# Performance work log

Hardware: AMD Instinct MI355X
Metric: run time of the kernel (lower is better)

Reference implementation:

```python
import jax, jax.numpy as jnp
import numpy as np

B, CIN, H, W = 4, 256, 64, 64
COUT = CIN // 2  # 128
EPS = 1e-5


def setup_inputs() -> dict:
    key = jax.random.key(0)
    ks = jax.random.split(key, 10)
    s_in = 1.0 / np.sqrt(CIN)
    s_out = 1.0 / np.sqrt(COUT)
    return {
        "x": jax.random.normal(ks[0], (B, CIN, H, W), dtype=jnp.float32),
        "Wq": jax.random.uniform(ks[1], (COUT, CIN), jnp.float32, -s_in, s_in),
        "bq": jax.random.uniform(ks[2], (COUT,), jnp.float32, -s_in, s_in),
        "Wk": jax.random.uniform(ks[3], (COUT, CIN), jnp.float32, -s_in, s_in),
        "bk": jax.random.uniform(ks[4], (COUT,), jnp.float32, -s_in, s_in),
        "Wv": jax.random.uniform(ks[5], (COUT, CIN), jnp.float32, -s_in, s_in),
        "bv": jax.random.uniform(ks[6], (COUT,), jnp.float32, -s_in, s_in),
        "Ww": jax.random.uniform(ks[7], (CIN, COUT), jnp.float32, -s_out, s_out),
        "bw": jax.random.uniform(ks[8], (CIN,), jnp.float32, -s_out, s_out),
        "bn_gamma": jnp.ones((CIN,), jnp.float32),
        "bn_beta": jnp.zeros((CIN,), jnp.float32),
        "bn_mean": jnp.zeros((CIN,), jnp.float32),
        "bn_var": jnp.ones((CIN,), jnp.float32),
    }


def reference(x, Wq, bq, Wk, bk, Wv, bv, Ww, bw, bn_gamma, bn_beta, bn_mean, bn_var):
    b, c, h, w = x.shape
    n = h * w
    xf = x.reshape(b, c, n)  # [B, Cin, N]
    # 1x1 convs == channel-mixing matmuls on flattened spatial dim
    q = jnp.einsum("oc,bcn->bon", Wq, xf) + bq[None, :, None]  # [B, Cout, N]
    k = jnp.einsum("oc,bcn->bon", Wk, xf) + bk[None, :, None]
    v = jnp.einsum("oc,bcn->bon", Wv, xf) + bv[None, :, None]
    # f = k^T @ q  (no scaling, as in the original)
    f = jnp.einsum("bcn,bcm->bnm", k, q)  # [B, N, N]
    f = jax.nn.softmax(f, axis=-1)
    # y = v @ f
    y = jnp.einsum("bcn,bnm->bcm", v, f)  # [B, Cout, N]
    # output 1x1 conv + eval-mode BatchNorm + residual
    z = jnp.einsum("oc,bcn->bon", Ww, y) + bw[None, :, None]  # [B, Cin, N]
    inv = bn_gamma / jnp.sqrt(bn_var + EPS)
    z = z * inv[None, :, None] + (bn_beta - bn_mean * inv)[None, :, None]
    return z.reshape(b, c, h, w) + x
```

## Files before the change

### kernel.cpp

```cpp
#include <hip/hip_runtime.h>
#include <hip/hip_bf16.h>

#define BATCH 4
#define CIN   256
#define CMID  128
#define NPOS  4096
#define EPS   1e-5f

typedef __bf16 bf16;
typedef __attribute__((ext_vector_type(8))) __bf16 bf16x8;
typedef __attribute__((ext_vector_type(4))) __bf16 bf16x4;
typedef __attribute__((ext_vector_type(4))) float  f32x4;

#define MFMA16(a, b, c) __builtin_amdgcn_mfma_f32_16x16x32_bf16((a), (b), (c), 0, 0, 0)

#define GLDS(gsrc, ldst) \
    __builtin_amdgcn_global_load_lds( \
        (const __attribute__((address_space(1))) void*)(gsrc), \
        (__attribute__((address_space(3))) void*)(ldst), 16, 0, 0)

__device__ __forceinline__ int swz128(int row, int colb) {
    return row * 128 + ((((colb >> 4) ^ (row & 7)) << 4) | (colb & 15));
}
__device__ __forceinline__ int swz256(int row, int colb) {
    return row * 256 + ((((colb >> 4) ^ (row & 7)) << 4) | (colb & 15));
}

__global__ __launch_bounds__(256) void kt_transpose(const float* __restrict__ x,
                                                    bf16* __restrict__ xT) {
    __shared__ float tile[64][65];
    int n0 = blockIdx.x * 64, c0 = blockIdx.y * 64, b = blockIdx.z;
    const float* xp = x + (size_t)b * CIN * NPOS;
    int t = threadIdx.x;
    int lr = t >> 4;
    int lc4 = (t & 15) * 4;
    for (int p = 0; p < 4; ++p) {
        int c = lr + p * 16;
        f32x4 v = *reinterpret_cast<const f32x4*>(xp + (size_t)(c0 + c) * NPOS + n0 + lc4);
        tile[c][lc4 + 0] = v[0]; tile[c][lc4 + 1] = v[1];
        tile[c][lc4 + 2] = v[2]; tile[c][lc4 + 3] = v[3];
    }
    __syncthreads();
    bf16* xtp = xT + (size_t)b * NPOS * CIN;
    int cc = (t & 15) * 4;
    for (int p = 0; p < 4; ++p) {
        int n = (t >> 4) + p * 16;
        bf16x4 o;
        o[0] = (bf16)tile[cc + 0][n]; o[1] = (bf16)tile[cc + 1][n];
        o[2] = (bf16)tile[cc + 2][n]; o[3] = (bf16)tile[cc + 3][n];
        *reinterpret_cast<bf16x4*>(xtp + (size_t)(n0 + n) * CIN + c0 + cc) = o;
    }
}

__global__ __launch_bounds__(256) void k_qkv(
    const float* __restrict__ Wq, const float* __restrict__ Wk, const float* __restrict__ Wv,
    const float* __restrict__ bq, const float* __restrict__ bk, const float* __restrict__ bv,
    const bf16* __restrict__ xT, bf16* __restrict__ qT, bf16* __restrict__ kT,
    bf16* __restrict__ vC) {
    __shared__ __align__(16) char a_lds[128 * 128];
    __shared__ __align__(16) char b_lds[128 * 128];
    int n0 = blockIdx.x * 128, which = blockIdx.y, b = blockIdx.z;
    const float* W    = which == 0 ? Wq : (which == 1 ? Wk : Wv);
    const float* bias = which == 0 ? bq : (which == 1 ? bk : bv);
    int t = threadIdx.x, lane = t & 63, w = t >> 6, wy = w >> 1, wx = w & 1;
    const bf16* xb = xT + (size_t)b * NPOS * CIN;

    f32x4 acc[4][4] = {};
    for (int k0 = 0; k0 < 256; k0 += 64) {
        __syncthreads();
        for (int i = 0; i < 8; ++i) {
            int idx = t + i * 256;
            int row = idx >> 4, c4 = (idx & 15) * 4;
            f32x4 v = *reinterpret_cast<const f32x4*>(W + (size_t)row * CIN + k0 + c4);
            bf16x4 o; o[0] = (bf16)v[0]; o[1] = (bf16)v[1]; o[2] = (bf16)v[2]; o[3] = (bf16)v[3];
            *reinterpret_cast<bf16x4*>(a_lds + swz128(row, c4 * 2)) = o;
        }
        for (int i = 0; i < 4; ++i) {
            int idx = t + i * 256;
            int row = idx >> 3, cb = (idx & 7) * 16;
            bf16x8 vv = *reinterpret_cast<const bf16x8*>(xb + (size_t)(n0 + row) * CIN + k0 + cb / 2);
            *reinterpret_cast<bf16x8*>(b_lds + swz128(row, cb)) = vv;
        }
        __syncthreads();
        for (int ks = 0; ks < 2; ++ks) {
            int kb = ks * 64 + (lane >> 4) * 16;
            bf16x8 af[4], bfr[4];
            for (int i = 0; i < 4; ++i)
                af[i] = *reinterpret_cast<const bf16x8*>(a_lds + swz128(wy * 64 + i * 16 + (lane & 15), kb));
            for (int j = 0; j < 4; ++j)
                bfr[j] = *reinterpret_cast<const bf16x8*>(b_lds + swz128(wx * 64 + j * 16 + (lane & 15), kb));
            for (int i = 0; i < 4; ++i)
                for (int j = 0; j < 4; ++j)
                    acc[i][j] = MFMA16(af[i], bfr[j], acc[i][j]);
        }
    }
    int rg = lane >> 4, cl = lane & 15;
    for (int i = 0; i < 4; ++i) {
        int ch0 = wy * 64 + i * 16 + rg * 4;
        f32x4 bv4 = *reinterpret_cast<const f32x4*>(bias + ch0);
        for (int j = 0; j < 4; ++j) {
            int n = n0 + wx * 64 + j * 16 + cl;
            f32x4 d = acc[i][j];
            for (int r = 0; r < 4; ++r) d[r] += bv4[r];
            if (which == 2) {
                for (int r = 0; r < 4; ++r)
                    vC[((size_t)b * CMID + ch0 + r) * NPOS + n] = (bf16)d[r];
            } else {
                bf16x4 o; o[0] = (bf16)d[0]; o[1] = (bf16)d[1]; o[2] = (bf16)d[2]; o[3] = (bf16)d[3];
                bf16* dst = (which == 0 ? qT : kT);
                *reinterpret_cast<bf16x4*>(dst + ((size_t)b * NPOS + n) * CMID + ch0) = o;
            }
        }
    }
}

__global__ __launch_bounds__(256, 4) void k_zrow(const bf16* __restrict__ qT,
                                                 const bf16* __restrict__ kT,
                                                 float* __restrict__ zpart) {
    __shared__ __align__(16) char q_lds[2][64 * 256];
    int n0 = blockIdx.x * 128, mq = blockIdx.y, b = blockIdx.z;
    int t = threadIdx.x, lane = t & 63, w = t >> 6;
    int cl = lane & 15, g = lane >> 4;
    const bf16* qb = qT + (size_t)b * NPOS * CMID;
    const bf16* kb = kT + (size_t)b * NPOS * CMID;

    auto stage_q = [&](int buf, int m0) {
        #pragma unroll
        for (int i = 0; i < 4; ++i) {
            int lc = (w * 4 + i) * 64 + lane;
            int r = lc >> 4, p = lc & 15;
            GLDS(qb + (size_t)(m0 + r) * CMID + ((p ^ (r & 7)) << 3),
                 q_lds[buf] + (w * 4 + i) * 1024);
        }
    };

    bf16x8 kreg[2][4];
    for (int jn = 0; jn < 2; ++jn)
        for (int ks = 0; ks < 4; ++ks)
            kreg[jn][ks] = *reinterpret_cast<const bf16x8*>(
                kb + (size_t)(n0 + w * 32 + jn * 16 + cl) * CMID + ks * 32 + g * 8);

    int mbeg = mq * (NPOS / 8);
    stage_q(0, mbeg);
    asm volatile("s_waitcnt vmcnt(0)" ::: "memory");
    __syncthreads();
    int cur = 0;
    float zacc[2] = {0.f, 0.f};
    for (int m0 = mbeg; m0 < mbeg + NPOS / 8; m0 += 64) {
        if (m0 + 64 < mbeg + NPOS / 8) stage_q(cur ^ 1, m0 + 64);
        f32x4 acc[4][2] = {};
        for (int ks = 0; ks < 4; ++ks) {
            bf16x8 qf[4];
            for (int im = 0; im < 4; ++im)
                qf[im] = *reinterpret_cast<const bf16x8*>(q_lds[cur] + swz256(im * 16 + cl, ks * 64 + g * 16));
            for (int im = 0; im < 4; ++im)
                for (int jn = 0; jn < 2; ++jn)
                    acc[im][jn] = MFMA16(qf[im], kreg[jn][ks], acc[im][jn]);
        }
        for (int im = 0; im < 4; ++im)
            for (int jn = 0; jn < 2; ++jn)
                for (int r = 0; r < 4; ++r)
                    zacc[jn] += __expf(acc[im][jn][r]);
        __syncthreads();
        cur ^= 1;
    }
    for (int jn = 0; jn < 2; ++jn) {
        zacc[jn] += __shfl_xor(zacc[jn], 16);
        zacc[jn] += __shfl_xor(zacc[jn], 32);
    }
    if (g == 0) {
        float* zp = zpart + ((size_t)mq * BATCH + b) * NPOS;
        zp[n0 + w * 32 + cl]      = zacc[0];
        zp[n0 + w * 32 + 16 + cl] = zacc[1];
    }
}

__global__ __launch_bounds__(256) void k_rcp(const float* __restrict__ zpart,
                                             float* __restrict__ invZ) {
    int i = (blockIdx.x * 256 + threadIdx.x) * 4;
    f32x4 s = {0.f, 0.f, 0.f, 0.f};
    for (int p = 0; p < 8; ++p) {
        f32x4 a = *reinterpret_cast<const f32x4*>(zpart + (size_t)p * BATCH * NPOS + i);
        for (int r = 0; r < 4; ++r) s[r] += a[r];
    }
    f32x4 o;
    for (int r = 0; r < 4; ++r) o[r] = 1.f / s[r];
    *reinterpret_cast<f32x4*>(invZ + i) = o;
}

__global__ __launch_bounds__(256) void k_vscale(bf16* __restrict__ vC,
                                                const float* __restrict__ invZ) {
    int idx = blockIdx.x * 256 + threadIdx.x;
    int b = idx >> 16;
    int n8 = idx & (NPOS / 8 - 1);
    bf16x8 v = *reinterpret_cast<const bf16x8*>(vC + (size_t)idx * 8);
    const float* iz = invZ + (size_t)b * NPOS + n8 * 8;
    f32x4 i0 = *reinterpret_cast<const f32x4*>(iz);
    f32x4 i1 = *reinterpret_cast<const f32x4*>(iz + 4);
    bf16x8 o;
    for (int r = 0; r < 4; ++r) {
        o[r]     = (bf16)((float)v[r]     * i0[r]);
        o[r + 4] = (bf16)((float)v[r + 4] * i1[r]);
    }
    *reinterpret_cast<bf16x8*>(vC + (size_t)idx * 8) = o;
}

__global__ __launch_bounds__(256, 2) void k_attn(const bf16* __restrict__ qT,
                                                 const bf16* __restrict__ kT,
                                                 const bf16* __restrict__ vS,
                                                 bf16* __restrict__ ypA,
                                                 bf16* __restrict__ ypB) {
    __shared__ __align__(16) char k_lds[2][64 * 256];
    __shared__ __align__(16) char v_lds[2][128 * 128];
    __shared__ __align__(16) char p_lds[128 * 128];
    int m0 = blockIdx.x * 128, nq = blockIdx.y, b = blockIdx.z;
    int t = threadIdx.x, lane = t & 63, w = t >> 6;
    int cl = lane & 15, g = lane >> 4;
    const bf16* qb = qT + (size_t)b * NPOS * CMID;
    const bf16* kb = kT + (size_t)b * NPOS * CMID;
    const bf16* vb = vS + (size_t)b * CMID * NPOS;

    auto stage_kv = [&](int buf, int n0) {
        #pragma unroll
        for (int i = 0; i < 4; ++i) {
            int lc = (w * 4 + i) * 64 + lane;
            int kr = lc >> 4, kp = lc & 15;
            GLDS(kb + (size_t)(n0 + kr) * CMID + ((kp ^ (kr & 7)) << 3),
                 k_lds[buf] + (w * 4 + i) * 1024);
            int vr = lc >> 3, vp = lc & 7;
            GLDS(vb + (size_t)vr * NPOS + n0 + ((vp ^ (vr & 7)) << 3),
                 v_lds[buf] + (w * 4 + i) * 1024);
        }
    };

    bf16x8 qreg[2][4];
    for (int jm = 0; jm < 2; ++jm)
        for (int ks = 0; ks < 4; ++ks)
            qreg[jm][ks] = *reinterpret_cast<const bf16x8*>(
                qb + (size_t)(m0 + w * 32 + jm * 16 + cl) * CMID + ks * 32 + g * 8);

    f32x4 acc2[2][8] = {};
    int nbeg = nq * (NPOS / 4);
    stage_kv(0, nbeg);
    asm volatile("s_waitcnt vmcnt(0)" ::: "memory");
    __syncthreads();
    int cur = 0;
    for (int s = 0; s < NPOS / 4 / 64; ++s) {
        int n0 = nbeg + s * 64;
        if (s + 1 < NPOS / 4 / 64) stage_kv(cur ^ 1, n0 + 64);
        f32x4 acc1[4][2] = {};
        for (int ks = 0; ks < 4; ++ks) {
            bf16x8 kf[4];
            for (int in = 0; in < 4; ++in)
                kf[in] = *reinterpret_cast<const bf16x8*>(k_lds[cur] + swz256(in * 16 + cl, ks * 64 + g * 16));
            for (int in = 0; in < 4; ++in)
                for (int jm = 0; jm < 2; ++jm)
                    acc1[in][jm] = MFMA16(kf[in], qreg[jm][ks], acc1[in][jm]);
        }
        for (int in = 0; in < 4; ++in)
            for (int jm = 0; jm < 2; ++jm) {
                bf16x4 o;
                for (int r = 0; r < 4; ++r) o[r] = (bf16)__expf(acc1[in][jm][r]);
                *reinterpret_cast<bf16x4*>(p_lds + swz128(w * 32 + jm * 16 + cl, in * 32 + g * 8)) = o;
            }
        for (int s32 = 0; s32 < 2; ++s32) {
            bf16x8 af[2], vf[8];
            for (int jm = 0; jm < 2; ++jm)
                af[jm] = *reinterpret_cast<const bf16x8*>(p_lds + swz128(w * 32 + jm * 16 + cl, s32 * 64 + g * 16));
            for (int j = 0; j < 8; ++j)
                vf[j] = *reinterpret_cast<const bf16x8*>(v_lds[cur] + swz128(j * 16 + cl, s32 * 64 + g * 16));
            for (int jm = 0; jm < 2; ++jm)
                for (int j = 0; j < 8; ++j)
                    acc2[jm][j] = MFMA16(af[jm], vf[j], acc2[jm][j]);
        }
        __syncthreads();
        cur ^= 1;
    }
    bf16* yb = ((nq & 2) ? ypB : ypA) + ((size_t)(nq & 1) * BATCH + b) * NPOS * CMID
             + (size_t)m0 * CMID;
    for (int jm = 0; jm < 2; ++jm)
        for (int j = 0; j < 8; ++j) {
            int c = j * 16 + cl;
            for (int r = 0; r < 4; ++r) {
                int m = w * 32 + jm * 16 + g * 4 + r;
                yb[(size_t)m * CMID + c] = (bf16)acc2[jm][j][r];
            }
        }
}

__global__ __launch_bounds__(256) void k_out(
    const float* __restrict__ Ww, const float* __restrict__ bw,
    const float* __restrict__ gamma, const float* __restrict__ beta,
    const float* __restrict__ mean, const float* __restrict__ var,
    const bf16* __restrict__ ypA, const bf16* __restrict__ ypB,
    const float* __restrict__ x, float* __restrict__ out) {
    __shared__ __align__(16) char a_lds[128 * 128];
    __shared__ __align__(16) char b_lds[128 * 128];
    int m0 = blockIdx.x * 128, o0 = blockIdx.y * 128, b = blockIdx.z;
    int t = threadIdx.x, lane = t & 63, w = t >> 6, wy = w >> 1, wx = w & 1;
    size_t boff = (size_t)b * NPOS * CMID;
    const bf16* y0 = ypA + boff;
    const bf16* y1 = ypA + (size_t)BATCH * NPOS * CMID + boff;
    const bf16* y2 = ypB + boff;
    const bf16* y3 = ypB + (size_t)BATCH * NPOS * CMID + boff;
    f32x4 acc[4][4] = {};
    for (int k0 = 0; k0 < 128; k0 += 64) {
        __syncthreads();
        for (int i = 0; i < 8; ++i) {
            int idx = t + i * 256, row = idx >> 4, c4 = (idx & 15) * 4;
            f32x4 v = *reinterpret_cast<const f32x4*>(Ww + (size_t)(o0 + row) * CMID + k0 + c4);
            bf16x4 o; o[0] = (bf16)v[0]; o[1] = (bf16)v[1]; o[2] = (bf16)v[2]; o[3] = (bf16)v[3];
            *reinterpret_cast<bf16x4*>(a_lds + swz128(row, c4 * 2)) = o;
        }
        for (int i = 0; i < 8; ++i) {
            int idx = t + i * 256, row = idx >> 4, c4 = (idx & 15) * 4;
            size_t yoff = (size_t)(m0 + row) * CMID + k0 + c4;
            bf16x4 a0 = *reinterpret_cast<const bf16x4*>(y0 + yoff);
            bf16x4 a1 = *reinterpret_cast<const bf16x4*>(y1 + yoff);
            bf16x4 a2 = *reinterpret_cast<const bf16x4*>(y2 + yoff);
            bf16x4 a3 = *reinterpret_cast<const bf16x4*>(y3 + yoff);
            bf16x4 o;
            for (int r = 0; r < 4; ++r)
                o[r] = (bf16)((float)a0[r] + (float)a1[r] + (float)a2[r] + (float)a3[r]);
            *reinterpret_cast<bf16x4*>(b_lds + swz128(row, c4 * 2)) = o;
        }
        __syncthreads();
        for (int ks = 0; ks < 2; ++ks) {
            int kb = ks * 64 + (lane >> 4) * 16;
            bf16x8 af[4], bfr[4];
            for (int i = 0; i < 4; ++i)
                af[i] = *reinterpret_cast<const bf16x8*>(a_lds + swz128(wy * 64 + i * 16 + (lane & 15), kb));
            for (int j = 0; j < 4; ++j)
                bfr[j] = *reinterpret_cast<const bf16x8*>(b_lds + swz128(wx * 64 + j * 16 + (lane & 15), kb));
            for (int i = 0; i < 4; ++i)
                for (int j = 0; j < 4; ++j)
                    acc[i][j] = MFMA16(af[i], bfr[j], acc[i][j]);
        }
    }
    int rg = lane >> 4, cl = lane & 15;
    const float* xb = x + (size_t)b * CIN * NPOS;
    float* ob = out + (size_t)b * CIN * NPOS;
    for (int i = 0; i < 4; ++i) {
        int och0 = o0 + wy * 64 + i * 16 + rg * 4;
        f32x4 g  = *reinterpret_cast<const f32x4*>(gamma + och0);
        f32x4 be = *reinterpret_cast<const f32x4*>(beta + och0);
        f32x4 mu = *reinterpret_cast<const f32x4*>(mean + och0);
        f32x4 va = *reinterpret_cast<const f32x4*>(var + och0);
        f32x4 bb = *reinterpret_cast<const f32x4*>(bw + och0);
        float invv[4], addv[4];
        for (int r = 0; r < 4; ++r) {
            invv[r] = g[r] / sqrtf(va[r] + EPS);
            addv[r] = be[r] - mu[r] * invv[r];
        }
        for (int j = 0; j < 4; ++j) {
            int m = m0 + wx * 64 + j * 16 + cl;
            for (int r = 0; r < 4; ++r) {
                float z = (acc[i][j][r] + bb[r]) * invv[r] + addv[r];
                ob[(size_t)(och0 + r) * NPOS + m] = z + xb[(size_t)(och0 + r) * NPOS + m];
            }
        }
    }
}

extern "C" void kernel_launch(void* const* d_in, const int* in_sizes, int n_in,
                              void* d_out, int out_size, void* d_ws, size_t ws_size,
                              hipStream_t stream) {
    const float* x     = (const float*)d_in[0];
    const float* Wq    = (const float*)d_in[1];
    const float* bq    = (const float*)d_in[2];
    const float* Wk    = (const float*)d_in[3];
    const float* bk    = (const float*)d_in[4];
    const float* Wv    = (const float*)d_in[5];
    const float* bv    = (const float*)d_in[6];
    const float* Ww    = (const float*)d_in[7];
    const float* bw    = (const float*)d_in[8];
    const float* gamma = (const float*)d_in[9];
    const float* beta  = (const float*)d_in[10];
    const float* mean  = (const float*)d_in[11];
    const float* var   = (const float*)d_in[12];
    float* out = (float*)d_out;

    char* ws = (char*)d_ws;
    char* regionA = ws;                    ws += (size_t)BATCH * NPOS * CIN * 2;
    bf16* qT = (bf16*)ws;                  ws += (size_t)BATCH * NPOS * CMID * 2;
    bf16* kT = (bf16*)ws;                  ws += (size_t)BATCH * NPOS * CMID * 2;
    bf16* vC = (bf16*)ws;                  ws += (size_t)BATCH * NPOS * CMID * 2;
    bf16* ypB = (bf16*)ws;                 ws += (size_t)2 * BATCH * NPOS * CMID * 2;
    float* zpart = (float*)ws;             ws += (size_t)8 * BATCH * NPOS * 4;
    float* invZ = (float*)ws;
    bf16* xT  = (bf16*)regionA;
    bf16* ypA = (bf16*)regionA;

    kt_transpose<<<dim3(NPOS / 64, CIN / 64, BATCH), 256, 0, stream>>>(x, xT);
    k_qkv<<<dim3(NPOS / 128, 3, BATCH), 256, 0, stream>>>(Wq, Wk, Wv, bq, bk, bv, xT, qT, kT, vC);
    k_zrow<<<dim3(NPOS / 128, 8, BATCH), 256, 0, stream>>>(qT, kT, zpart);
    k_rcp<<<dim3(BATCH * NPOS / 1024), 256, 0, stream>>>(zpart, invZ);
    k_vscale<<<dim3(BATCH * CMID * NPOS / 8 / 256), 256, 0, stream>>>(vC, invZ);
    k_attn<<<dim3(NPOS / 128, 4, BATCH), 256, 0, stream>>>(qT, kT, vC, ypA, ypB);
    k_out<<<dim3(NPOS / 128, 2, BATCH), 256, 0, stream>>>(Ww, bw, gamma, beta, mean, var, ypA, ypB, x, out);
}
```

Measured before the change: 99.81 us.

## Triple-buffer K/V and Q tiles with 32-row stages and finer output tiling

The zrow and attention kernels move from double-buffered 64-row stages to triple-buffered 32-row stages. Each stage waits with a partial vmcnt and a single barrier, and the MFMA sections run at raised priority through setprio. The V tile layout and the P scratch layout change to a 4-chunk XOR swizzle that matches the 32-wide K step. The output kernel uses 64-column tiles, which doubles the grid for better occupancy. The smaller stages add more barriers and loop iterations, and LDS per block shrinks.

```diff
diff --git a/kernel.cpp b/kernel.cpp
--- a/kernel.cpp
+++ b/kernel.cpp
@@ -19,11 +19,16 @@
         (const __attribute__((address_space(1))) void*)(gsrc), \
         (__attribute__((address_space(3))) void*)(ldst), 16, 0, 0)
 
+#define WAITVM(N) asm volatile("s_waitcnt vmcnt(" #N ")" ::: "memory")
+
+__device__ __forceinline__ int swz256(int row, int colb) {
+    return row * 256 + ((((colb >> 4) ^ (row & 7)) << 4) | (colb & 15));
+}
 __device__ __forceinline__ int swz128(int row, int colb) {
     return row * 128 + ((((colb >> 4) ^ (row & 7)) << 4) | (colb & 15));
 }
-__device__ __forceinline__ int swz256(int row, int colb) {
-    return row * 256 + ((((colb >> 4) ^ (row & 7)) << 4) | (colb & 15));
+__device__ __forceinline__ int cswz(int row, int n4) {
+    return (row * 4 + (n4 ^ ((row >> 1) & 3))) * 16;
 }
 
 __global__ __launch_bounds__(256) void kt_transpose(const float* __restrict__ x,
@@ -117,7 +122,7 @@
 __global__ __launch_bounds__(256, 4) void k_zrow(const bf16* __restrict__ qT,
                                                  const bf16* __restrict__ kT,
                                                  float* __restrict__ zpart) {
-    __shared__ __align__(16) char q_lds[2][64 * 256];
+    __shared__ __align__(16) char q_lds[3 * 8192];
     int n0 = blockIdx.x * 128, mq = blockIdx.y, b = blockIdx.z;
     int t = threadIdx.x, lane = t & 63, w = t >> 6;
     int cl = lane & 15, g = lane >> 4;
@@ -126,11 +131,11 @@
 
     auto stage_q = [&](int buf, int m0) {
         #pragma unroll
-        for (int i = 0; i < 4; ++i) {
-            int lc = (w * 4 + i) * 64 + lane;
+        for (int i = 0; i < 2; ++i) {
+            int lc = (w * 2 + i) * 64 + lane;
             int r = lc >> 4, p = lc & 15;
             GLDS(qb + (size_t)(m0 + r) * CMID + ((p ^ (r & 7)) << 3),
-                 q_lds[buf] + (w * 4 + i) * 1024);
+                 q_lds + buf * 8192 + (w * 2 + i) * 1024);
         }
     };
 
@@ -142,27 +147,34 @@
 
     int mbeg = mq * (NPOS / 8);
     stage_q(0, mbeg);
-    asm volatile("s_waitcnt vmcnt(0)" ::: "memory");
-    __syncthreads();
-    int cur = 0;
+    stage_q(1, mbeg + 32);
+    const int NS = (NPOS / 8) / 32;
+    int cur = 0, nxt = 2;
     float zacc[2] = {0.f, 0.f};
-    for (int m0 = mbeg; m0 < mbeg + NPOS / 8; m0 += 64) {
-        if (m0 + 64 < mbeg + NPOS / 8) stage_q(cur ^ 1, m0 + 64);
-        f32x4 acc[4][2] = {};
+    for (int s = 0; s < NS; ++s) {
+        if (s < NS - 1) { WAITVM(2); } else { WAITVM(0); }
+        asm volatile("" ::: "memory");
+        __builtin_amdgcn_s_barrier();
+        asm volatile("" ::: "memory");
+        if (s + 2 < NS) stage_q(nxt, mbeg + (s + 2) * 32);
+        const char* qbuf = q_lds + cur * 8192;
+        f32x4 acc[2][2] = {};
+        __builtin_amdgcn_s_setprio(1);
         for (int ks = 0; ks < 4; ++ks) {
-            bf16x8 qf[4];
-            for (int im = 0; im < 4; ++im)
-                qf[im] = *reinterpret_cast<const bf16x8*>(q_lds[cur] + swz256(im * 16 + cl, ks * 64 + g * 16));
-            for (int im = 0; im < 4; ++im)
+            bf16x8 qf[2];
+            for (int im = 0; im < 2; ++im)
+                qf[im] = *reinterpret_cast<const bf16x8*>(qbuf + swz256(im * 16 + cl, ks * 64 + g * 16));
+            for (int im = 0; im < 2; ++im)
                 for (int jn = 0; jn < 2; ++jn)
                     acc[im][jn] = MFMA16(qf[im], kreg[jn][ks], acc[im][jn]);
         }
-        for (int im = 0; im < 4; ++im)
+        __builtin_amdgcn_s_setprio(0);
+        for (int im = 0; im < 2; ++im)
             for (int jn = 0; jn < 2; ++jn)
                 for (int r = 0; r < 4; ++r)
                     zacc[jn] += __expf(acc[im][jn][r]);
-        __syncthreads();
-        cur ^= 1;
+        cur = (cur == 2) ? 0 : cur + 1;
+        nxt = (nxt == 2) ? 0 : nxt + 1;
     }
     for (int jn = 0; jn < 2; ++jn) {
         zacc[jn] += __shfl_xor(zacc[jn], 16);
@@ -210,9 +222,9 @@
                                                  const bf16* __restrict__ vS,
                                                  bf16* __restrict__ ypA,
                                                  bf16* __restrict__ ypB) {
-    __shared__ __align__(16) char k_lds[2][64 * 256];
-    __shared__ __align__(16) char v_lds[2][128 * 128];
-    __shared__ __align__(16) char p_lds[128 * 128];
+    __shared__ __align__(16) char k_lds[3 * 8192];
+    __shared__ __align__(16) char v_lds[3 * 8192];
+    __shared__ __align__(16) char p_lds[8192];
     int m0 = blockIdx.x * 128, nq = blockIdx.y, b = blockIdx.z;
     int t = threadIdx.x, lane = t & 63, w = t >> 6;
     int cl = lane & 15, g = lane >> 4;
@@ -222,14 +234,15 @@
 
     auto stage_kv = [&](int buf, int n0) {
         #pragma unroll
-        for (int i = 0; i < 4; ++i) {
-            int lc = (w * 4 + i) * 64 + lane;
+        for (int i = 0; i < 2; ++i) {
+            int lc = (w * 2 + i) * 64 + lane;
             int kr = lc >> 4, kp = lc & 15;
             GLDS(kb + (size_t)(n0 + kr) * CMID + ((kp ^ (kr & 7)) << 3),
-                 k_lds[buf] + (w * 4 + i) * 1024);
-            int vr = lc >> 3, vp = lc & 7;
-            GLDS(vb + (size_t)vr * NPOS + n0 + ((vp ^ (vr & 7)) << 3),
-                 v_lds[buf] + (w * 4 + i) * 1024);
+                 k_lds + buf * 8192 + (w * 2 + i) * 1024);
+            int vc = lc >> 2;
+            int vn4 = (lc & 3) ^ ((vc >> 1) & 3);
+            GLDS(vb + (size_t)vc * NPOS + n0 + vn4 * 8,
+                 v_lds + buf * 8192 + (w * 2 + i) * 1024);
         }
     };
 
@@ -242,39 +255,48 @@
     f32x4 acc2[2][8] = {};
     int nbeg = nq * (NPOS / 4);
     stage_kv(0, nbeg);
-    asm volatile("s_waitcnt vmcnt(0)" ::: "memory");
-    __syncthreads();
-    int cur = 0;
-    for (int s = 0; s < NPOS / 4 / 64; ++s) {
-        int n0 = nbeg + s * 64;
-        if (s + 1 < NPOS / 4 / 64) stage_kv(cur ^ 1, n0 + 64);
-        f32x4 acc1[4][2] = {};
+    stage_kv(1, nbeg + 32);
+    const int NS = (NPOS / 4) / 32;
+    int cur = 0, nxt = 2;
+    for (int s = 0; s < NS; ++s) {
+        int n0 = nbeg + s * 32;
+        if (s < NS - 1) { WAITVM(4); } else { WAITVM(0); }
+        asm volatile("" ::: "memory");
+        __builtin_amdgcn_s_barrier();
+        asm volatile("" ::: "memory");
+        if (s + 2 < NS) stage_kv(nxt, n0 + 64);
+        const char* kbuf = k_lds + cur * 8192;
+        const char* vbuf = v_lds + cur * 8192;
+        f32x4 acc1[2][2] = {};
+        __builtin_amdgcn_s_setprio(1);
         for (int ks = 0; ks < 4; ++ks) {
-            bf16x8 kf[4];
-            for (int in = 0; in < 4; ++in)
-                kf[in] = *reinterpret_cast<const bf16x8*>(k_lds[cur] + swz256(in * 16 + cl, ks * 64 + g * 16));
-            for (int in = 0; in < 4; ++in)
+            bf16x8 kf[2];
+            for (int in = 0; in < 2; ++in)
+                kf[in] = *reinterpret_cast<const bf16x8*>(kbuf + swz256(in * 16 + cl, ks * 64 + g * 16));
+            for (int in = 0; in < 2; ++in)
                 for (int jm = 0; jm < 2; ++jm)
                     acc1[in][jm] = MFMA16(kf[in], qreg[jm][ks], acc1[in][jm]);
         }
-        for (int in = 0; in < 4; ++in)
+        __builtin_amdgcn_s_setprio(0);
+        for (int in = 0; in < 2; ++in)
             for (int jm = 0; jm < 2; ++jm) {
+                int m = w * 32 + jm * 16 + cl;
                 bf16x4 o;
                 for (int r = 0; r < 4; ++r) o[r] = (bf16)__expf(acc1[in][jm][r]);
-                *reinterpret_cast<bf16x4*>(p_lds + swz128(w * 32 + jm * 16 + cl, in * 32 + g * 8)) = o;
+                *reinterpret_cast<bf16x4*>(p_lds + cswz(m, in * 2 + (g >> 1)) + (g & 1) * 8) = o;
             }
-        for (int s32 = 0; s32 < 2; ++s32) {
-            bf16x8 af[2], vf[8];
+        bf16x8 af[2];
+        for (int jm = 0; jm < 2; ++jm)
+            af[jm] = *reinterpret_cast<const bf16x8*>(p_lds + cswz(w * 32 + jm * 16 + cl, g));
+        __builtin_amdgcn_s_setprio(1);
+        for (int j = 0; j < 8; ++j) {
+            bf16x8 vf = *reinterpret_cast<const bf16x8*>(vbuf + cswz(j * 16 + cl, g));
             for (int jm = 0; jm < 2; ++jm)
-                af[jm] = *reinterpret_cast<const bf16x8*>(p_lds + swz128(w * 32 + jm * 16 + cl, s32 * 64 + g * 16));
-            for (int j = 0; j < 8; ++j)
-                vf[j] = *reinterpret_cast<const bf16x8*>(v_lds[cur] + swz128(j * 16 + cl, s32 * 64 + g * 16));
-            for (int jm = 0; jm < 2; ++jm)
-                for (int j = 0; j < 8; ++j)
-                    acc2[jm][j] = MFMA16(af[jm], vf[j], acc2[jm][j]);
-        }
-        __syncthreads();
-        cur ^= 1;
+                acc2[jm][j] = MFMA16(af[jm], vf, acc2[jm][j]);
+        }
+        __builtin_amdgcn_s_setprio(0);
+        cur = (cur == 2) ? 0 : cur + 1;
+        nxt = (nxt == 2) ? 0 : nxt + 1;
     }
     bf16* yb = ((nq & 2) ? ypB : ypA) + ((size_t)(nq & 1) * BATCH + b) * NPOS * CMID
              + (size_t)m0 * CMID;
@@ -295,15 +317,15 @@
     const bf16* __restrict__ ypA, const bf16* __restrict__ ypB,
     const float* __restrict__ x, float* __restrict__ out) {
     __shared__ __align__(16) char a_lds[128 * 128];
-    __shared__ __align__(16) char b_lds[128 * 128];
-    int m0 = blockIdx.x * 128, o0 = blockIdx.y * 128, b = blockIdx.z;
+    __shared__ __align__(16) char b_lds[64 * 128];
+    int m0 = blockIdx.x * 64, o0 = blockIdx.y * 128, b = blockIdx.z;
     int t = threadIdx.x, lane = t & 63, w = t >> 6, wy = w >> 1, wx = w & 1;
     size_t boff = (size_t)b * NPOS * CMID;
     const bf16* y0 = ypA + boff;
     const bf16* y1 = ypA + (size_t)BATCH * NPOS * CMID + boff;
     const bf16* y2 = ypB + boff;
     const bf16* y3 = ypB + (size_t)BATCH * NPOS * CMID + boff;
-    f32x4 acc[4][4] = {};
+    f32x4 acc[4][2] = {};
     for (int k0 = 0; k0 < 128; k0 += 64) {
         __syncthreads();
         for (int i = 0; i < 8; ++i) {
@@ -312,7 +334,7 @@
             bf16x4 o; o[0] = (bf16)v[0]; o[1] = (bf16)v[1]; o[2] = (bf16)v[2]; o[3] = (bf16)v[3];
             *reinterpret_cast<bf16x4*>(a_lds + swz128(row, c4 * 2)) = o;
         }
-        for (int i = 0; i < 8; ++i) {
+        for (int i = 0; i < 4; ++i) {
             int idx = t + i * 256, row = idx >> 4, c4 = (idx & 15) * 4;
             size_t yoff = (size_t)(m0 + row) * CMID + k0 + c4;
             bf16x4 a0 = *reinterpret_cast<const bf16x4*>(y0 + yoff);
@@ -327,13 +349,13 @@
         __syncthreads();
         for (int ks = 0; ks < 2; ++ks) {
             int kb = ks * 64 + (lane >> 4) * 16;
-            bf16x8 af[4], bfr[4];
+            bf16x8 af[4], bfr[2];
             for (int i = 0; i < 4; ++i)
                 af[i] = *reinterpret_cast<const bf16x8*>(a_lds + swz128(wy * 64 + i * 16 + (lane & 15), kb));
-            for (int j = 0; j < 4; ++j)
-                bfr[j] = *reinterpret_cast<const bf16x8*>(b_lds + swz128(wx * 64 + j * 16 + (lane & 15), kb));
+            for (int j = 0; j < 2; ++j)
+                bfr[j] = *reinterpret_cast<const bf16x8*>(b_lds + swz128(wx * 32 + j * 16 + (lane & 15), kb));
             for (int i = 0; i < 4; ++i)
-                for (int j = 0; j < 4; ++j)
+                for (int j = 0; j < 2; ++j)
                     acc[i][j] = MFMA16(af[i], bfr[j], acc[i][j]);
         }
     }
@@ -342,18 +364,18 @@
     float* ob = out + (size_t)b * CIN * NPOS;
     for (int i = 0; i < 4; ++i) {
         int och0 = o0 + wy * 64 + i * 16 + rg * 4;
-        f32x4 g  = *reinterpret_cast<const f32x4*>(gamma + och0);
+        f32x4 gg = *reinterpret_cast<const f32x4*>(gamma + och0);
         f32x4 be = *reinterpret_cast<const f32x4*>(beta + och0);
         f32x4 mu = *reinterpret_cast<const f32x4*>(mean + och0);
         f32x4 va = *reinterpret_cast<const f32x4*>(var + och0);
         f32x4 bb = *reinterpret_cast<const f32x4*>(bw + och0);
         float invv[4], addv[4];
         for (int r = 0; r < 4; ++r) {
-            invv[r] = g[r] / sqrtf(va[r] + EPS);
+            invv[r] = gg[r] / sqrtf(va[r] + EPS);
             addv[r] = be[r] - mu[r] * invv[r];
         }
-        for (int j = 0; j < 4; ++j) {
-            int m = m0 + wx * 64 + j * 16 + cl;
+        for (int j = 0; j < 2; ++j) {
+            int m = m0 + wx * 32 + j * 16 + cl;
             for (int r = 0; r < 4; ++r) {
                 float z = (acc[i][j][r] + bb[r]) * invv[r] + addv[r];
                 ob[(size_t)(och0 + r) * NPOS + m] = z + xb[(size_t)(och0 + r) * NPOS + m];
@@ -397,5 +419,5 @@
     k_rcp<<<dim3(BATCH * NPOS / 1024), 256, 0, stream>>>(zpart, invZ);
     k_vscale<<<dim3(BATCH * CMID * NPOS / 8 / 256), 256, 0, stream>>>(vC, invZ);
     k_attn<<<dim3(NPOS / 128, 4, BATCH), 256, 0, stream>>>(qT, kT, vC, ypA, ypB);
-    k_out<<<dim3(NPOS / 128, 2, BATCH), 256, 0, stream>>>(Ww, bw, gamma, beta, mean, var, ypA, ypB, x, out);
-}
+    k_out<<<dim3(NPOS / 64, 2, BATCH), 256, 0, stream>>>(Ww, bw, gamma, beta, mean, var, ypA, ypB, x, out);
+}
```

Result: slower. 102.6 us (+2.8%).

## Shrink attention LDS for higher occupancy, widen split-K, retile output GEMM

Applied to the files above, without the earlier changes.

The attention kernel drops double-buffered K/V staging and shrinks the P tile to 64 columns, processed in two halves, to cut LDS use. Launch bounds rise to 4 blocks per CU, aiming for more resident waves to hide latency instead of explicit prefetch. The key-dimension split goes from 4 to 8 when the workspace is large enough, giving more blocks. The output kernel now sums a variable number of partial slices and uses 64-column tiles for more parallelism, at the cost of extra partial traffic and a synchronous load per step.

```diff
diff --git a/kernel.cpp b/kernel.cpp
--- a/kernel.cpp
+++ b/kernel.cpp
@@ -19,11 +19,14 @@
         (const __attribute__((address_space(1))) void*)(gsrc), \
         (__attribute__((address_space(3))) void*)(ldst), 16, 0, 0)
 
+__device__ __forceinline__ int swz256(int row, int colb) {
+    return row * 256 + ((((colb >> 4) ^ (row & 7)) << 4) | (colb & 15));
+}
 __device__ __forceinline__ int swz128(int row, int colb) {
     return row * 128 + ((((colb >> 4) ^ (row & 7)) << 4) | (colb & 15));
 }
-__device__ __forceinline__ int swz256(int row, int colb) {
-    return row * 256 + ((((colb >> 4) ^ (row & 7)) << 4) | (colb & 15));
+__device__ __forceinline__ int cswz(int row, int n4) {
+    return (row * 4 + (n4 ^ ((row >> 1) & 3))) * 16;
 }
 
 __global__ __launch_bounds__(256) void kt_transpose(const float* __restrict__ x,
@@ -205,79 +208,77 @@
     *reinterpret_cast<bf16x8*>(vC + (size_t)idx * 8) = o;
 }
 
-__global__ __launch_bounds__(256, 2) void k_attn(const bf16* __restrict__ qT,
+__global__ __launch_bounds__(256, 4) void k_attn(const bf16* __restrict__ qT,
                                                  const bf16* __restrict__ kT,
                                                  const bf16* __restrict__ vS,
-                                                 bf16* __restrict__ ypA,
-                                                 bf16* __restrict__ ypB) {
-    __shared__ __align__(16) char k_lds[2][64 * 256];
-    __shared__ __align__(16) char v_lds[2][128 * 128];
-    __shared__ __align__(16) char p_lds[128 * 128];
+                                                 bf16* __restrict__ ys) {
+    __shared__ __align__(16) char k_lds[64 * 256];
+    __shared__ __align__(16) char v_lds[128 * 128];
+    __shared__ __align__(16) char p_lds[128 * 64];
     int m0 = blockIdx.x * 128, nq = blockIdx.y, b = blockIdx.z;
+    int nqn = NPOS / gridDim.y;
     int t = threadIdx.x, lane = t & 63, w = t >> 6;
     int cl = lane & 15, g = lane >> 4;
     const bf16* qb = qT + (size_t)b * NPOS * CMID;
     const bf16* kb = kT + (size_t)b * NPOS * CMID;
     const bf16* vb = vS + (size_t)b * CMID * NPOS;
 
-    auto stage_kv = [&](int buf, int n0) {
+    bf16x8 qreg[2][4];
+    for (int jm = 0; jm < 2; ++jm)
+        for (int ks = 0; ks < 4; ++ks)
+            qreg[jm][ks] = *reinterpret_cast<const bf16x8*>(
+                qb + (size_t)(m0 + w * 32 + jm * 16 + cl) * CMID + ks * 32 + g * 8);
+
+    f32x4 acc2[2][8] = {};
+    int nbeg = nq * nqn;
+    for (int s = 0; s < nqn / 64; ++s) {
+        int n0 = nbeg + s * 64;
+        __syncthreads();
         #pragma unroll
         for (int i = 0; i < 4; ++i) {
             int lc = (w * 4 + i) * 64 + lane;
             int kr = lc >> 4, kp = lc & 15;
             GLDS(kb + (size_t)(n0 + kr) * CMID + ((kp ^ (kr & 7)) << 3),
-                 k_lds[buf] + (w * 4 + i) * 1024);
+                 k_lds + (w * 4 + i) * 1024);
             int vr = lc >> 3, vp = lc & 7;
             GLDS(vb + (size_t)vr * NPOS + n0 + ((vp ^ (vr & 7)) << 3),
-                 v_lds[buf] + (w * 4 + i) * 1024);
-        }
-    };
-
-    bf16x8 qreg[2][4];
-    for (int jm = 0; jm < 2; ++jm)
-        for (int ks = 0; ks < 4; ++ks)
-            qreg[jm][ks] = *reinterpret_cast<const bf16x8*>(
-                qb + (size_t)(m0 + w * 32 + jm * 16 + cl) * CMID + ks * 32 + g * 8);
-
-    f32x4 acc2[2][8] = {};
-    int nbeg = nq * (NPOS / 4);
-    stage_kv(0, nbeg);
-    asm volatile("s_waitcnt vmcnt(0)" ::: "memory");
-    __syncthreads();
-    int cur = 0;
-    for (int s = 0; s < NPOS / 4 / 64; ++s) {
-        int n0 = nbeg + s * 64;
-        if (s + 1 < NPOS / 4 / 64) stage_kv(cur ^ 1, n0 + 64);
+                 v_lds + (w * 4 + i) * 1024);
+        }
+        asm volatile("s_waitcnt vmcnt(0)" ::: "memory");
+        __syncthreads();
         f32x4 acc1[4][2] = {};
         for (int ks = 0; ks < 4; ++ks) {
             bf16x8 kf[4];
             for (int in = 0; in < 4; ++in)
-                kf[in] = *reinterpret_cast<const bf16x8*>(k_lds[cur] + swz256(in * 16 + cl, ks * 64 + g * 16));
+                kf[in] = *reinterpret_cast<const bf16x8*>(k_lds + swz256(in * 16 + cl, ks * 64 + g * 16));
             for (int in = 0; in < 4; ++in)
                 for (int jm = 0; jm < 2; ++jm)
                     acc1[in][jm] = MFMA16(kf[in], qreg[jm][ks], acc1[in][jm]);
         }
-        for (int in = 0; in < 4; ++in)
-            for (int jm = 0; jm < 2; ++jm) {
-                bf16x4 o;
-                for (int r = 0; r < 4; ++r) o[r] = (bf16)__expf(acc1[in][jm][r]);
-                *reinterpret_cast<bf16x4*>(p_lds + swz128(w * 32 + jm * 16 + cl, in * 32 + g * 8)) = o;
+        #pragma unroll
+        for (int ih = 0; ih < 2; ++ih) {
+            #pragma unroll
+            for (int in2 = 0; in2 < 2; ++in2)
+                #pragma unroll
+                for (int jm = 0; jm < 2; ++jm) {
+                    int m = w * 32 + jm * 16 + cl;
+                    bf16x4 o;
+                    for (int r = 0; r < 4; ++r)
+                        o[r] = (bf16)__expf(acc1[ih * 2 + in2][jm][r]);
+                    *reinterpret_cast<bf16x4*>(p_lds + cswz(m, in2 * 2 + (g >> 1)) + (g & 1) * 8) = o;
+                }
+            bf16x8 af[2];
+            for (int jm = 0; jm < 2; ++jm)
+                af[jm] = *reinterpret_cast<const bf16x8*>(p_lds + cswz(w * 32 + jm * 16 + cl, g));
+            for (int j = 0; j < 8; ++j) {
+                bf16x8 vf = *reinterpret_cast<const bf16x8*>(v_lds + swz128(j * 16 + cl, ih * 64 + g * 16));
+                for (int jm = 0; jm < 2; ++jm)
+                    acc2[jm][j] = MFMA16(af[jm], vf, acc2[jm][j]);
             }
-        for (int s32 = 0; s32 < 2; ++s32) {
-            bf16x8 af[2], vf[8];
-            for (int jm = 0; jm < 2; ++jm)
-                af[jm] = *reinterpret_cast<const bf16x8*>(p_lds + swz128(w * 32 + jm * 16 + cl, s32 * 64 + g * 16));
-            for (int j = 0; j < 8; ++j)
-                vf[j] = *reinterpret_cast<const bf16x8*>(v_lds[cur] + swz128(j * 16 + cl, s32 * 64 + g * 16));
-            for (int jm = 0; jm < 2; ++jm)
-                for (int j = 0; j < 8; ++j)
-                    acc2[jm][j] = MFMA16(af[jm], vf[j], acc2[jm][j]);
-        }
-        __syncthreads();
-        cur ^= 1;
-    }
-    bf16* yb = ((nq & 2) ? ypB : ypA) + ((size_t)(nq & 1) * BATCH + b) * NPOS * CMID
-             + (size_t)m0 * CMID;
+        }
+    }
+    bf16* yb = ys + (size_t)nq * BATCH * NPOS * CMID
+             + ((size_t)b * NPOS + m0) * CMID;
     for (int jm = 0; jm < 2; ++jm)
         for (int j = 0; j < 8; ++j) {
             int c = j * 16 + cl;
@@ -292,18 +293,14 @@
     const float* __restrict__ Ww, const float* __restrict__ bw,
     const float* __restrict__ gamma, const float* __restrict__ beta,
     const float* __restrict__ mean, const float* __restrict__ var,
-    const bf16* __restrict__ ypA, const bf16* __restrict__ ypB,
+    const bf16* __restrict__ ys, int ns,
     const float* __restrict__ x, float* __restrict__ out) {
     __shared__ __align__(16) char a_lds[128 * 128];
-    __shared__ __align__(16) char b_lds[128 * 128];
-    int m0 = blockIdx.x * 128, o0 = blockIdx.y * 128, b = blockIdx.z;
+    __shared__ __align__(16) char b_lds[64 * 128];
+    int m0 = blockIdx.x * 64, o0 = blockIdx.y * 128, b = blockIdx.z;
     int t = threadIdx.x, lane = t & 63, w = t >> 6, wy = w >> 1, wx = w & 1;
-    size_t boff = (size_t)b * NPOS * CMID;
-    const bf16* y0 = ypA + boff;
-    const bf16* y1 = ypA + (size_t)BATCH * NPOS * CMID + boff;
-    const bf16* y2 = ypB + boff;
-    const bf16* y3 = ypB + (size_t)BATCH * NPOS * CMID + boff;
-    f32x4 acc[4][4] = {};
+    const size_t SL = (size_t)BATCH * NPOS * CMID;
+    f32x4 acc[4][2] = {};
     for (int k0 = 0; k0 < 128; k0 += 64) {
         __syncthreads();
         for (int i = 0; i < 8; ++i) {
@@ -312,28 +309,28 @@
             bf16x4 o; o[0] = (bf16)v[0]; o[1] = (bf16)v[1]; o[2] = (bf16)v[2]; o[3] = (bf16)v[3];
             *reinterpret_cast<bf16x4*>(a_lds + swz128(row, c4 * 2)) = o;
         }
-        for (int i = 0; i < 8; ++i) {
+        for (int i = 0; i < 4; ++i) {
             int idx = t + i * 256, row = idx >> 4, c4 = (idx & 15) * 4;
-            size_t yoff = (size_t)(m0 + row) * CMID + k0 + c4;
-            bf16x4 a0 = *reinterpret_cast<const bf16x4*>(y0 + yoff);
-            bf16x4 a1 = *reinterpret_cast<const bf16x4*>(y1 + yoff);
-            bf16x4 a2 = *reinterpret_cast<const bf16x4*>(y2 + yoff);
-            bf16x4 a3 = *reinterpret_cast<const bf16x4*>(y3 + yoff);
+            size_t yoff = ((size_t)b * NPOS + m0 + row) * CMID + k0 + c4;
+            float sacc[4] = {0.f, 0.f, 0.f, 0.f};
+            for (int p = 0; p < ns; ++p) {
+                bf16x4 a = *reinterpret_cast<const bf16x4*>(ys + (size_t)p * SL + yoff);
+                for (int r = 0; r < 4; ++r) sacc[r] += (float)a[r];
+            }
             bf16x4 o;
-            for (int r = 0; r < 4; ++r)
-                o[r] = (bf16)((float)a0[r] + (float)a1[r] + (float)a2[r] + (float)a3[r]);
+            for (int r = 0; r < 4; ++r) o[r] = (bf16)sacc[r];
             *reinterpret_cast<bf16x4*>(b_lds + swz128(row, c4 * 2)) = o;
         }
         __syncthreads();
         for (int ks = 0; ks < 2; ++ks) {
             int kb = ks * 64 + (lane >> 4) * 16;
-            bf16x8 af[4], bfr[4];
+            bf16x8 af[4], bfr[2];
             for (int i = 0; i < 4; ++i)
                 af[i] = *reinterpret_cast<const bf16x8*>(a_lds + swz128(wy * 64 + i * 16 + (lane & 15), kb));
-            for (int j = 0; j < 4; ++j)
-                bfr[j] = *reinterpret_cast<const bf16x8*>(b_lds + swz128(wx * 64 + j * 16 + (lane & 15), kb));
+            for (int j = 0; j < 2; ++j)
+                bfr[j] = *reinterpret_cast<const bf16x8*>(b_lds + swz128(wx * 32 + j * 16 + (lane & 15), kb));
             for (int i = 0; i < 4; ++i)
-                for (int j = 0; j < 4; ++j)
+                for (int j = 0; j < 2; ++j)
                     acc[i][j] = MFMA16(af[i], bfr[j], acc[i][j]);
         }
     }
@@ -342,18 +339,18 @@
     float* ob = out + (size_t)b * CIN * NPOS;
     for (int i = 0; i < 4; ++i) {
         int och0 = o0 + wy * 64 + i * 16 + rg * 4;
-        f32x4 g  = *reinterpret_cast<const f32x4*>(gamma + och0);
+        f32x4 gg = *reinterpret_cast<const f32x4*>(gamma + och0);
         f32x4 be = *reinterpret_cast<const f32x4*>(beta + och0);
         f32x4 mu = *reinterpret_cast<const f32x4*>(mean + och0);
         f32x4 va = *reinterpret_cast<const f32x4*>(var + och0);
         f32x4 bb = *reinterpret_cast<const f32x4*>(bw + och0);
         float invv[4], addv[4];
         for (int r = 0; r < 4; ++r) {
-            invv[r] = g[r] / sqrtf(va[r] + EPS);
+            invv[r] = gg[r] / sqrtf(va[r] + EPS);
             addv[r] = be[r] - mu[r] * invv[r];
         }
-        for (int j = 0; j < 4; ++j) {
-            int m = m0 + wx * 64 + j * 16 + cl;
+        for (int j = 0; j < 2; ++j) {
+            int m = m0 + wx * 32 + j * 16 + cl;
             for (int r = 0; r < 4; ++r) {
                 float z = (acc[i][j][r] + bb[r]) * invv[r] + addv[r];
                 ob[(size_t)(och0 + r) * NPOS + m] = z + xb[(size_t)(och0 + r) * NPOS + m];
@@ -380,22 +377,25 @@
     const float* var   = (const float*)d_in[12];
     float* out = (float*)d_out;
 
-    char* ws = (char*)d_ws;
-    char* regionA = ws;                    ws += (size_t)BATCH * NPOS * CIN * 2;
-    bf16* qT = (bf16*)ws;                  ws += (size_t)BATCH * NPOS * CMID * 2;
-    bf16* kT = (bf16*)ws;                  ws += (size_t)BATCH * NPOS * CMID * 2;
-    bf16* vC = (bf16*)ws;                  ws += (size_t)BATCH * NPOS * CMID * 2;
-    bf16* ypB = (bf16*)ws;                 ws += (size_t)2 * BATCH * NPOS * CMID * 2;
-    float* zpart = (float*)ws;             ws += (size_t)8 * BATCH * NPOS * 4;
-    float* invZ = (float*)ws;
-    bf16* xT  = (bf16*)regionA;
-    bf16* ypA = (bf16*)regionA;
+    const size_t slice = (size_t)BATCH * NPOS * CMID * 2;
+    const size_t zbytes = (size_t)8 * BATCH * NPOS * 4 + (size_t)BATCH * NPOS * 4;
+    const size_t need8 = 8 * slice + 3 * slice + zbytes;
+    const int NQ = (ws_size >= need8) ? 8 : 4;
+
+    char* p = (char*)d_ws;
+    bf16* ys = (bf16*)p;        p += (size_t)NQ * slice;
+    bf16* qT = (bf16*)p;        p += slice;
+    bf16* kT = (bf16*)p;        p += slice;
+    bf16* vC = (bf16*)p;        p += slice;
+    float* zpart = (float*)p;   p += (size_t)8 * BATCH * NPOS * 4;
+    float* invZ = (float*)p;
+    bf16* xT = (bf16*)d_ws;
 
     kt_transpose<<<dim3(NPOS / 64, CIN / 64, BATCH), 256, 0, stream>>>(x, xT);
     k_qkv<<<dim3(NPOS / 128, 3, BATCH), 256, 0, stream>>>(Wq, Wk, Wv, bq, bk, bv, xT, qT, kT, vC);
     k_zrow<<<dim3(NPOS / 128, 8, BATCH), 256, 0, stream>>>(qT, kT, zpart);
     k_rcp<<<dim3(BATCH * NPOS / 1024), 256, 0, stream>>>(zpart, invZ);
     k_vscale<<<dim3(BATCH * CMID * NPOS / 8 / 256), 256, 0, stream>>>(vC, invZ);
-    k_attn<<<dim3(NPOS / 128, 4, BATCH), 256, 0, stream>>>(qT, kT, vC, ypA, ypB);
-    k_out<<<dim3(NPOS / 128, 2, BATCH), 256, 0, stream>>>(Ww, bw, gamma, beta, mean, var, ypA, ypB, x, out);
-}
+    k_attn<<<dim3(NPOS / 128, NQ, BATCH), 256, 0, stream>>>(qT, kT, vC, ys);
+    k_out<<<dim3(NPOS / 64, 2, BATCH), 256, 0, stream>>>(Ww, bw, gamma, beta, mean, var, ys, NQ, x, out);
+}
```

New measurement: 148.9 us. +49.2%, slower.
